# Kernel optimization log

Measured on AMD Instinct MI355X. Metric: run time of the kernel, lower is better.

Reference implementation:

```python
import jax, jax.numpy as jnp
import numpy as np

B, C, H, W = 4, 96, 56, 56
K0, K1, DIL, HID = 5, 7, 3, 4  # HID: ConvMlp(dim, expansion, drop) => hidden_features = int(mlp_ratio) = 4 (repo quirk)
EPS = 1e-5


def _conv(x, w, b, pad, dil=1, groups=1):
    y = jax.lax.conv_general_dilated(x, w, (1, 1), [(pad, pad), (pad, pad)],
                                     rhs_dilation=(dil, dil),
                                     dimension_numbers=('NCHW', 'OIHW', 'NCHW'),
                                     feature_group_count=groups)
    return y + b[None, :, None, None]


def _conv1x1(x, w, b):
    return jnp.einsum('bchw,oc->bohw', x, w) + b[None, :, None, None]


def _ln(x, g, b):
    # LayerNormProxy: LayerNorm over channel dim of NCHW
    mu = jnp.mean(x, axis=1, keepdims=True)
    v = jnp.var(x, axis=1, keepdims=True)
    return (x - mu) * jax.lax.rsqrt(v + EPS) * g[None, :, None, None] + b[None, :, None, None]


def _gelu(x):
    return jax.nn.gelu(x, approximate=False)  # torch nn.GELU default = exact erf


def _deform_dw(x, ow, ob, dw, db, k, dil, pad):
    # DeformConv2d wrapper: offsets from a same-geometry conv, then depthwise deformable conv.
    Bx, Cx, Hx, Wx = x.shape
    P = k * k
    off = _conv(x, ow, ob, pad, dil).reshape(Bx, P, 2, Hx, Wx)  # [B,P,(y,x),H,W]
    ky = (jnp.repeat(jnp.arange(k), k) * dil - pad).astype(x.dtype)  # row-major kernel grid
    kx = (jnp.tile(jnp.arange(k), k) * dil - pad).astype(x.dtype)
    py = jnp.arange(Hx, dtype=x.dtype)[None, None, :, None] + ky[None, :, None, None] + off[:, :, 0]
    px = jnp.arange(Wx, dtype=x.dtype)[None, None, None, :] + kx[None, :, None, None] + off[:, :, 1]
    y0 = jnp.floor(py)
    x0 = jnp.floor(px)
    wy = py - y0
    wx = px - x0
    xf = x.reshape(Bx, Cx, Hx * Wx)

    def corner(yi, xi):
        valid = (yi >= 0) & (yi < Hx) & (xi >= 0) & (xi < Wx)
        idx = (jnp.clip(yi, 0, Hx - 1).astype(jnp.int32) * Wx
               + jnp.clip(xi, 0, Wx - 1).astype(jnp.int32)).reshape(Bx, -1)
        g = jax.vmap(lambda a, i: jnp.take(a, i, axis=1))(xf, idx).reshape(Bx, Cx, P, Hx, Wx)
        return g * valid[:, None].astype(x.dtype)

    v = (corner(y0, x0) * ((1 - wy) * (1 - wx))[:, None]
         + corner(y0, x0 + 1) * ((1 - wy) * wx)[:, None]
         + corner(y0 + 1, x0) * (wy * (1 - wx))[:, None]
         + corner(y0 + 1, x0 + 1) * (wy * wx)[:, None])  # [B,C,P,H,W]
    return jnp.einsum('bcphw,cp->bchw', v, dw) + db[None, :, None, None]


def setup_inputs() -> dict:
    key = jax.random.key(0)
    ks = iter(jax.random.split(key, 32))

    def rn(shape, s=1.0):
        return jax.random.normal(next(ks), shape, jnp.float32) * s

    f32 = jnp.float32
    return {
        'x': rn((B, C, H, W)),
        'g1n': jnp.ones((C,), f32), 'b1n': jnp.zeros((C,), f32),
        'p1w': rn((C, C), 1 / np.sqrt(C)), 'p1b': jnp.zeros((C,), f32),
        'o0w': rn((2 * K0 * K0, C, K0, K0), 0.05 / np.sqrt(C * K0 * K0)), 'o0b': jnp.zeros((2 * K0 * K0,), f32),
        'd0w': rn((C, K0 * K0), 1 / np.sqrt(K0 * K0)), 'd0b': jnp.zeros((C,), f32),
        'o1w': rn((2 * K1 * K1, C, K1, K1), 0.05 / np.sqrt(C * K1 * K1)), 'o1b': jnp.zeros((2 * K1 * K1,), f32),
        'd1w': rn((C, K1 * K1), 1 / np.sqrt(K1 * K1)), 'd1b': jnp.zeros((C,), f32),
        'c1w': rn((C, C), 1 / np.sqrt(C)), 'c1b': jnp.zeros((C,), f32),
        'p2w': rn((C, C), 1 / np.sqrt(C)), 'p2b': jnp.zeros((C,), f32),
        'ls1': jnp.full((C,), 0.01, f32),
        'g2n': jnp.ones((C,), f32), 'b2n': jnp.zeros((C,), f32),
        'f1w': rn((HID, C), 1 / np.sqrt(C)), 'f1b': jnp.zeros((HID,), f32),
        'dww': rn((HID, 1, 3, 3), 1 / 3.0), 'dwb': jnp.zeros((HID,), f32),
        'f2w': rn((C, HID), 1 / np.sqrt(HID)), 'f2b': jnp.zeros((C,), f32),
        'ls2': jnp.full((C,), 0.01, f32),
    }


def reference(x, g1n, b1n, p1w, p1b, o0w, o0b, d0w, d0b, o1w, o1b, d1w, d1b,
              c1w, c1b, p2w, p2b, ls1, g2n, b2n, f1w, f1b, dww, dwb, f2w, f2b, ls2):
    # attention branch
    y = _ln(x, g1n, b1n)
    shortcut = y
    y = _gelu(_conv1x1(y, p1w, p1b))
    u = y
    a = _deform_dw(y, o0w, o0b, d0w, d0b, K0, 1, K0 // 2)
    a = _deform_dw(a, o1w, o1b, d1w, d1b, K1, DIL, (K1 // 2) * DIL)
    a = _conv1x1(a, c1w, c1b)
    y = _conv1x1(u * a, p2w, p2b) + shortcut
    y = ls1[None, :, None, None] * y
    x = x + y
    # MLP branch (note: norm2 is applied to the branch output y, as in the source)
    z = _ln(y, g2n, b2n)
    z = _conv1x1(z, f1w, f1b)
    z = _gelu(_conv(z, dww, dwb, 1, 1, HID))
    z = _conv1x1(z, f2w, f2b)
    x = x + ls2[None, :, None, None] * z
    return x
```

## Files before the change

kernel.cpp:

```cpp
#include <hip/hip_runtime.h>
#include <math.h>

namespace {

constexpr int Bc = 4, Cc = 96, Hc = 56, Wc = 56;
constexpr int HWc = Hc * Wc;
constexpr int Nc  = Bc * HWc;
constexpr float EPSc = 1e-5f;

typedef __attribute__((ext_vector_type(8))) short bf16x8;
typedef __attribute__((ext_vector_type(4))) float f32x4;

__device__ __forceinline__ unsigned short f2bf(float f) {
  union { float f; unsigned u; } x; x.f = f;
  unsigned r = x.u + 0x7fffu + ((x.u >> 16) & 1u);
  return (unsigned short)(r >> 16);
}
__device__ __forceinline__ float bf2f(unsigned short u) {
  union { unsigned u; float f; } x; x.u = (unsigned)u << 16; return x.f;
}
__device__ __forceinline__ float gelu_exact(float x) {
  return 0.5f * x * (1.0f + erff(x * 0.7071067811865475f));
}

__global__ __launch_bounds__(256) void k_ln(const float* __restrict__ x,
                                            const float* __restrict__ g,
                                            const float* __restrict__ b,
                                            unsigned short* __restrict__ outN) {
  int pos = blockIdx.x * 256 + threadIdx.x;
  int bb = pos / HWc, hw = pos % HWc;
  const float* xb = x + (size_t)bb * Cc * HWc + hw;
  float s = 0.f, s2 = 0.f;
  for (int c = 0; c < Cc; ++c) { float v = xb[c * HWc]; s += v; s2 += v * v; }
  float mu  = s * (1.f / Cc);
  float var = fmaxf(s2 * (1.f / Cc) - mu * mu, 0.f);
  float rs  = rsqrtf(var + EPSc);
  unsigned short* ob = outN + (size_t)pos * Cc;
  for (int q = 0; q < 12; ++q) {
    unsigned short t8[8];
#pragma unroll
    for (int j = 0; j < 8; ++j) {
      int c = q * 8 + j;
      t8[j] = f2bf((xb[c * HWc] - mu) * rs * g[c] + b[c]);
    }
    *reinterpret_cast<bf16x8*>(ob + q * 8) = *reinterpret_cast<const bf16x8*>(t8);
  }
}

template <int K_, int MTILES, int P>
__global__ __launch_bounds__(256) void k_pack_w(const float* __restrict__ wsrc,
                                                unsigned short* __restrict__ wpk) {
  constexpr int TOTAL = K_ * K_ * 3 * MTILES * 512;
  int idx = blockIdx.x * 256 + threadIdx.x;
  if (idx >= TOTAL) return;
  int j    = idx & 7;
  int lane = (idx >> 3) & 63;
  int t    = idx >> 9;
  int mt   = t % MTILES;
  int step = t / MTILES;
  int o = mt * 16 + (lane & 15);
  int k = step * 32 + ((lane >> 4) & 3) * 8 + j;
  int p = k / Cc, c = k % Cc;
  float v = 0.f;
  if (o < P) v = wsrc[(((size_t)o * Cc + c) * K_ + p / K_) * K_ + (p % K_)];
  wpk[idx] = f2bf(v);
}

__global__ __launch_bounds__(256) void k_pack_dwt(const float* __restrict__ dwsrc,
                                                  float* __restrict__ dwt, int KK) {
  int idx = blockIdx.x * 256 + threadIdx.x;
  if (idx >= KK * Cc) return;
  int p = idx / Cc, c = idx % Cc;
  dwt[idx] = dwsrc[c * KK + p];
}

template <int GELU, int PADP, int WP>
__global__ __launch_bounds__(256) void k_pwg(const unsigned short* __restrict__ inN,
                                             const unsigned short* __restrict__ wpk,
                                             const float* __restrict__ bq,
                                             unsigned short* __restrict__ outPad) {
  int lane = threadIdx.x & 63;
  int wv = threadIdx.x >> 6;
  int ng = wv & 1, mg = wv >> 1;
  int n = blockIdx.x * 32 + ng * 16 + (lane & 15);
  int ko = ((lane >> 4) & 3) * 8;
  const unsigned short* ib = inN + (size_t)n * Cc + ko;
  const unsigned short* wl = wpk + (size_t)lane * 8;
  f32x4 acc[3];
#pragma unroll
  for (int m = 0; m < 3; ++m) acc[m] = (f32x4){0.f, 0.f, 0.f, 0.f};
#pragma unroll
  for (int ks = 0; ks < 3; ++ks) {
    bf16x8 bf = *reinterpret_cast<const bf16x8*>(ib + ks * 32);
#pragma unroll
    for (int m = 0; m < 3; ++m) {
      bf16x8 af = *reinterpret_cast<const bf16x8*>(wl + (size_t)(ks * 6 + mg * 3 + m) * 512);
      acc[m] = __builtin_amdgcn_mfma_f32_16x16x32_bf16(af, bf, acc[m], 0, 0, 0);
    }
  }
  int bb = n / HWc, hw = n % HWc;
  int h = hw / Wc, w = hw % Wc;
  unsigned short* ob = outPad + (((size_t)bb * (Hc + 2 * PADP) + h + PADP) * WP + w + PADP) * Cc;
  int orow = ((lane >> 4) & 3) * 4;
#pragma unroll
  for (int m = 0; m < 3; ++m) {
    int o0 = (mg * 3 + m) * 16 + orow;
    float4 bv = *reinterpret_cast<const float4*>(bq + o0);
    unsigned short t4[4];
#pragma unroll
    for (int j = 0; j < 4; ++j) {
      float r = acc[m][j] + ((const float*)&bv)[j];
      if (GELU) r = gelu_exact(r);
      t4[j] = f2bf(r);
    }
    *reinterpret_cast<uint2*>(ob + o0) = *reinterpret_cast<const uint2*>(t4);
  }
}

template <int UPADP, int UWP>
__global__ __launch_bounds__(256) void k_comb(const unsigned short* __restrict__ uPad,
                                              const unsigned short* __restrict__ An,
                                              const unsigned short* __restrict__ wpk,
                                              const float* __restrict__ bq,
                                              const unsigned short* __restrict__ ylnN,
                                              const float* __restrict__ ls1q,
                                              const float* __restrict__ x,
                                              float* __restrict__ out,
                                              unsigned short* __restrict__ y2N) {
  int lane = threadIdx.x & 63;
  int wv = threadIdx.x >> 6;
  int ng = wv & 1, mg = wv >> 1;
  int n = blockIdx.x * 32 + ng * 16 + (lane & 15);
  int ko = ((lane >> 4) & 3) * 8;
  int bb = n / HWc, hw = n % HWc;
  int h = hw / Wc, w = hw % Wc;
  const unsigned short* ub = uPad + (((size_t)bb * (Hc + 2 * UPADP) + h + UPADP) * UWP + w + UPADP) * Cc + ko;
  const unsigned short* ab = An + (size_t)n * Cc + ko;
  const unsigned short* wl = wpk + (size_t)lane * 8;
  f32x4 acc[3];
#pragma unroll
  for (int m = 0; m < 3; ++m) acc[m] = (f32x4){0.f, 0.f, 0.f, 0.f};
#pragma unroll
  for (int ks = 0; ks < 3; ++ks) {
    bf16x8 uv = *reinterpret_cast<const bf16x8*>(ub + ks * 32);
    bf16x8 av = *reinterpret_cast<const bf16x8*>(ab + ks * 32);
    union { bf16x8 v; unsigned short s[8]; } uu, aa, gg;
    uu.v = uv; aa.v = av;
#pragma unroll
    for (int j = 0; j < 8; ++j) gg.s[j] = f2bf(bf2f(uu.s[j]) * bf2f(aa.s[j]));
#pragma unroll
    for (int m = 0; m < 3; ++m) {
      bf16x8 af = *reinterpret_cast<const bf16x8*>(wl + (size_t)(ks * 6 + mg * 3 + m) * 512);
      acc[m] = __builtin_amdgcn_mfma_f32_16x16x32_bf16(af, gg.v, acc[m], 0, 0, 0);
    }
  }
  int orow = ((lane >> 4) & 3) * 4;
  const float* xb = x + (size_t)bb * Cc * HWc + hw;
  float* ob = out + (size_t)bb * Cc * HWc + hw;
#pragma unroll
  for (int m = 0; m < 3; ++m) {
    int o0 = (mg * 3 + m) * 16 + orow;
    float4 bv = *reinterpret_cast<const float4*>(bq + o0);
    float4 lv = *reinterpret_cast<const float4*>(ls1q + o0);
    uint2 yl = *reinterpret_cast<const uint2*>(ylnN + (size_t)n * Cc + o0);
    unsigned short yl4[4];
    *reinterpret_cast<uint2*>(yl4) = yl;
    unsigned short t4[4];
#pragma unroll
    for (int j = 0; j < 4; ++j) {
      float t = acc[m][j] + ((const float*)&bv)[j] + bf2f(yl4[j]);
      float y2 = ((const float*)&lv)[j] * t;
      t4[j] = f2bf(y2);
      ob[(size_t)(o0 + j) * HWc] = xb[(size_t)(o0 + j) * HWc] + y2;
    }
    *reinterpret_cast<uint2*>(y2N + (size_t)n * Cc + o0) = *reinterpret_cast<const uint2*>(t4);
  }
}

template <int K_, int DIL_, int MTILES, int MT, int P, int PADP, int WP, int PSTR, int SPLIT>
__global__ __launch_bounds__(256) void k_conv_mfma(const unsigned short* __restrict__ inp,
                                                   const unsigned short* __restrict__ wpk,
                                                   const float* __restrict__ bq,
                                                   float* __restrict__ dstT) {
  constexpr int KK = K_ * K_;
  constexpr int KKbase = KK / SPLIT, KKrem = KK % SPLIT;
  constexpr int HP = Hc + 2 * PADP;
  constexpr int NBLK = Nc / 32;
  int lane = threadIdx.x & 63;
  int wv = threadIdx.x >> 6;
  int bid = blockIdx.x;
  int sp = blockIdx.y;
  int p0 = sp * KKbase + min(sp, KKrem);
  int pcnt = KKbase + (sp < KKrem ? 1 : 0);
  int ntile = (bid & 7) * (NBLK / 8) + (bid >> 3);
  int n0 = ntile * 32 + (lane & 15);
  int n1 = n0 + 16;
  int b0 = n0 / HWc, hw0 = n0 % HWc, h0 = hw0 / Wc, w0 = hw0 % Wc;
  int b1 = n1 / HWc, hw1 = n1 % HWc, h1 = hw1 / Wc, w1 = hw1 % Wc;
  int co = ((lane >> 4) & 3) * 8;
  const unsigned short* ib0 = inp + ((size_t)b0 * HP * WP + (size_t)h0 * WP + w0) * Cc + co;
  const unsigned short* ib1 = inp + ((size_t)b1 * HP * WP + (size_t)h1 * WP + w1) * Cc + co;
  const unsigned short* wl = wpk + (size_t)lane * 8;
  int mt0 = wv * MT;
  int mtc[MT];
#pragma unroll
  for (int i = 0; i < MT; ++i) mtc[i] = min(mt0 + i, MTILES - 1);

  f32x4 acc[MT][2];
#pragma unroll
  for (int i = 0; i < MT; ++i) {
    acc[i][0] = (f32x4){0.f, 0.f, 0.f, 0.f};
    acc[i][1] = (f32x4){0.f, 0.f, 0.f, 0.f};
  }

  bf16x8 Bb[3][2], Aa[MT][3];
  {
    size_t toff = (size_t)((p0 / K_) * DIL_ * WP + (p0 % K_) * DIL_) * Cc;
#pragma unroll
    for (int cc = 0; cc < 3; ++cc) {
      Bb[cc][0] = *reinterpret_cast<const bf16x8*>(ib0 + toff + cc * 32);
      Bb[cc][1] = *reinterpret_cast<const bf16x8*>(ib1 + toff + cc * 32);
#pragma unroll
      for (int i = 0; i < MT; ++i)
        Aa[i][cc] = *reinterpret_cast<const bf16x8*>(wl + ((size_t)(p0 * 3 + cc) * MTILES + mtc[i]) * 512);
    }
  }

#pragma unroll 2
  for (int pi = 0; pi < pcnt; ++pi) {
    int pn = p0 + ((pi + 1 < pcnt) ? pi + 1 : pi);
    size_t toff = (size_t)((pn / K_) * DIL_ * WP + (pn % K_) * DIL_) * Cc;
    const unsigned short* sp0 = ib0 + toff;
    const unsigned short* sp1 = ib1 + toff;
    bf16x8 Bn[3][2], An[MT][3];
#pragma unroll
    for (int cc = 0; cc < 3; ++cc) {
      Bn[cc][0] = *reinterpret_cast<const bf16x8*>(sp0 + cc * 32);
      Bn[cc][1] = *reinterpret_cast<const bf16x8*>(sp1 + cc * 32);
#pragma unroll
      for (int i = 0; i < MT; ++i)
        An[i][cc] = *reinterpret_cast<const bf16x8*>(wl + ((size_t)(pn * 3 + cc) * MTILES + mtc[i]) * 512);
    }
#pragma unroll
    for (int cc = 0; cc < 3; ++cc)
#pragma unroll
      for (int i = 0; i < MT; ++i) {
        acc[i][0] = __builtin_amdgcn_mfma_f32_16x16x32_bf16(Aa[i][cc], Bb[cc][0], acc[i][0], 0, 0, 0);
        acc[i][1] = __builtin_amdgcn_mfma_f32_16x16x32_bf16(Aa[i][cc], Bb[cc][1], acc[i][1], 0, 0, 0);
      }
#pragma unroll
    for (int cc = 0; cc < 3; ++cc) {
      Bb[cc][0] = Bn[cc][0];
      Bb[cc][1] = Bn[cc][1];
#pragma unroll
      for (int i = 0; i < MT; ++i) Aa[i][cc] = An[i][cc];
    }
  }

  float* dsp = dstT + (size_t)sp * Nc * PSTR;
  int orow = ((lane >> 4) & 3) * 4;
#pragma unroll
  for (int i = 0; i < MT; ++i) {
    int mt = mt0 + i;
    if (mt >= MTILES) break;
#pragma unroll
    for (int nt = 0; nt < 2; ++nt) {
      float4 st;
#pragma unroll
      for (int j = 0; j < 4; ++j) {
        int o = mt * 16 + orow + j;
        float bias = (sp == 0 && o < P) ? bq[o] : 0.f;
        ((float*)&st)[j] = acc[i][nt][j] + bias;
      }
      int n = nt ? n1 : n0;
      *reinterpret_cast<float4*>(dsp + (size_t)n * PSTR + mt * 16 + orow) = st;
    }
  }
}

template <int K_, int DIL_, int PAD_, int PSTR, int NSUM>
__global__ __launch_bounds__(256) void k_meta(const float* __restrict__ offT,
                                              uint2* __restrict__ metaI,
                                              float4* __restrict__ metaW) {
  constexpr int KK = K_ * K_;
  int idx = blockIdx.x * 256 + threadIdx.x;
  if (idx >= Nc * KK) return;
  int p = idx % KK, pos = idx / KK;
  int hw = pos % HWc;
  int h = hw / Wc, w = hw % Wc;
  const float* ob = offT + (size_t)pos * PSTR + 2 * p;
  float oy = ob[0], ox = ob[1];
#pragma unroll
  for (int q = 1; q < NSUM; ++q) {
    oy += ob[(size_t)q * Nc * PSTR];
    ox += ob[(size_t)q * Nc * PSTR + 1];
  }
  float py = (float)(h + (p / K_) * DIL_ - PAD_) + oy;
  float px = (float)(w + (p % K_) * DIL_ - PAD_) + ox;
  float y0f = floorf(py), x0f = floorf(px);
  float wy = py - y0f, wx = px - x0f;
  int y0 = (int)y0f, x0 = (int)x0f;
  int y1 = y0 + 1, x1 = x0 + 1;
  bool y0v = (unsigned)y0 < (unsigned)Hc, y1v = (unsigned)y1 < (unsigned)Hc;
  bool x0v = (unsigned)x0 < (unsigned)Wc, x1v = (unsigned)x1 < (unsigned)Wc;
  int y0c = min(max(y0, 0), Hc - 1), y1c = min(max(y1, 0), Hc - 1);
  int x0c = min(max(x0, 0), Wc - 1), x1c = min(max(x1, 0), Wc - 1);
  uint2 mi;
  mi.x = (unsigned)(y0c | (y1c << 16));
  mi.y = (unsigned)(x0c | (x1c << 16));
  float4 mw;
  mw.x = (y0v && x0v) ? (1.f - wy) * (1.f - wx) : 0.f;
  mw.y = (y0v && x1v) ? (1.f - wy) * wx : 0.f;
  mw.z = (y1v && x0v) ? wy * (1.f - wx) : 0.f;
  mw.w = (y1v && x1v) ? wy * wx : 0.f;
  metaI[idx] = mi;
  metaW[idx] = mw;
}

template <int K_, int IPADP, int IWP, int OPADP, int OWP>
__global__ __launch_bounds__(256) void k_deform2(const unsigned short* __restrict__ srcT,
                                                 const uint2* __restrict__ metaI,
                                                 const float4* __restrict__ metaW,
                                                 const float* __restrict__ dwt,
                                                 const float* __restrict__ dbq,
                                                 unsigned short* __restrict__ dstPad) {
  constexpr int KK = K_ * K_;
  constexpr int IHP = Hc + 2 * IPADP;
  int tid = blockIdx.x * 256 + threadIdx.x;
  int cg = tid % 12;
  int pos = tid / 12;
  int c = cg * 8;
  int bb = pos / HWc, hw = pos % HWc;
  int h = hw / Wc, w = hw % Wc;
  const unsigned short* sb = srcT + (size_t)bb * IHP * IWP * Cc + c;
  const uint2* mi = metaI + (size_t)pos * KK;
  const float4* mw = metaW + (size_t)pos * KK;
  float acc[8];
#pragma unroll
  for (int j = 0; j < 8; ++j) acc[j] = 0.f;

  auto tap = [&](int p, uint2 I, float4 W) {
    int y0 = (int)(I.x & 0xffffu) + IPADP, y1 = (int)(I.x >> 16) + IPADP;
    int x0 = (int)(I.y & 0xffffu) + IPADP, x1 = (int)(I.y >> 16) + IPADP;
    int r0 = y0 * IWP, r1 = y1 * IWP;
    const uint4 v00 = *reinterpret_cast<const uint4*>(sb + (size_t)(r0 + x0) * Cc);
    const uint4 v01 = *reinterpret_cast<const uint4*>(sb + (size_t)(r0 + x1) * Cc);
    const uint4 v10 = *reinterpret_cast<const uint4*>(sb + (size_t)(r1 + x0) * Cc);
    const uint4 v11 = *reinterpret_cast<const uint4*>(sb + (size_t)(r1 + x1) * Cc);
    float4 d0 = *reinterpret_cast<const float4*>(dwt + (size_t)p * Cc + c);
    float4 d1 = *reinterpret_cast<const float4*>(dwt + (size_t)p * Cc + c + 4);
    float dv[8] = {d0.x, d0.y, d0.z, d0.w, d1.x, d1.y, d1.z, d1.w};
#pragma unroll
    for (int j = 0; j < 4; ++j) {
      unsigned u00 = ((const unsigned*)&v00)[j], u01 = ((const unsigned*)&v01)[j];
      unsigned u10 = ((const unsigned*)&v10)[j], u11 = ((const unsigned*)&v11)[j];
      union { unsigned u; float f; } a0_, b0_, a1_, b1_, a2_, b2_, a3_, b3_;
      a0_.u = u00 << 16; b0_.u = u00 & 0xffff0000u;
      a1_.u = u01 << 16; b1_.u = u01 & 0xffff0000u;
      a2_.u = u10 << 16; b2_.u = u10 & 0xffff0000u;
      a3_.u = u11 << 16; b3_.u = u11 & 0xffff0000u;
      float lo = W.x * a0_.f + W.y * a1_.f + W.z * a2_.f + W.w * a3_.f;
      float hi = W.x * b0_.f + W.y * b1_.f + W.z * b2_.f + W.w * b3_.f;
      acc[2 * j]     += lo * dv[2 * j];
      acc[2 * j + 1] += hi * dv[2 * j + 1];
    }
  };

  int p = 0;
  for (; p + 1 < KK; p += 2) {
    uint2 I0 = mi[p], I1 = mi[p + 1];
    float4 W0 = mw[p], W1 = mw[p + 1];
    tap(p, I0, W0);
    tap(p + 1, I1, W1);
  }
  { uint2 I = mi[p]; float4 W = mw[p]; tap(p, I, W); }

  unsigned short t8[8];
#pragma unroll
  for (int j = 0; j < 8; ++j) t8[j] = f2bf(acc[j] + dbq[c + j]);
  unsigned short* tb = dstPad + (((size_t)bb * (Hc + 2 * OPADP) + h + OPADP) * OWP + w + OPADP) * Cc + c;
  *reinterpret_cast<bf16x8*>(tb) = *reinterpret_cast<const bf16x8*>(t8);
}

__global__ __launch_bounds__(256) void k_mlp1(const unsigned short* __restrict__ y2N,
                                              const float* __restrict__ g,
                                              const float* __restrict__ b,
                                              const float* __restrict__ f1wq,
                                              const float* __restrict__ f1bq,
                                              float* __restrict__ z4) {
  int pos = blockIdx.x * 256 + threadIdx.x;
  int bb = pos / HWc, hw = pos % HWc;
  const unsigned short* yb = y2N + (size_t)pos * Cc;
  float vv[96];
  float s = 0.f, s2 = 0.f;
#pragma unroll
  for (int q = 0; q < 12; ++q) {
    bf16x8 t = *reinterpret_cast<const bf16x8*>(yb + q * 8);
    union { bf16x8 v; unsigned short s[8]; } u; u.v = t;
#pragma unroll
    for (int j = 0; j < 8; ++j) {
      float f = bf2f(u.s[j]);
      vv[q * 8 + j] = f; s += f; s2 += f * f;
    }
  }
  float mu  = s * (1.f / Cc);
  float var = fmaxf(s2 * (1.f / Cc) - mu * mu, 0.f);
  float rs  = rsqrtf(var + EPSc);
  float a0 = 0.f, a1 = 0.f, a2 = 0.f, a3 = 0.f;
#pragma unroll
  for (int c = 0; c < 96; ++c) {
    float t = (vv[c] - mu) * rs * g[c] + b[c];
    a0 += t * f1wq[0 * Cc + c];
    a1 += t * f1wq[1 * Cc + c];
    a2 += t * f1wq[2 * Cc + c];
    a3 += t * f1wq[3 * Cc + c];
  }
  float* zb = z4 + (size_t)bb * 4 * HWc + hw;
  zb[0 * HWc] = a0 + f1bq[0];
  zb[1 * HWc] = a1 + f1bq[1];
  zb[2 * HWc] = a2 + f1bq[2];
  zb[3 * HWc] = a3 + f1bq[3];
}

__global__ __launch_bounds__(256) void k_mlp_dw(const float* __restrict__ z4,
                                                const float* __restrict__ dwwq,
                                                const float* __restrict__ dwbq,
                                                float* __restrict__ z4b) {
  int tid = blockIdx.x * 256 + threadIdx.x;
  int hw = tid % HWc;
  int bj = tid / HWc;
  int j = bj % 4;
  int h = hw / Wc, w = hw % Wc;
  const float* zb = z4 + (size_t)bj * HWc;
  float s = 0.f;
#pragma unroll
  for (int ky = 0; ky < 3; ++ky) {
    int y = h + ky - 1;
    if ((unsigned)y >= (unsigned)Hc) continue;
#pragma unroll
    for (int kx = 0; kx < 3; ++kx) {
      int x = w + kx - 1;
      if ((unsigned)x >= (unsigned)Wc) continue;
      s += zb[y * Wc + x] * dwwq[j * 9 + ky * 3 + kx];
    }
  }
  z4b[tid] = gelu_exact(s + dwbq[j]);
}

__global__ __launch_bounds__(256) void k_mlp2(const float* __restrict__ z4b,
                                              const float* __restrict__ f2wq,
                                              const float* __restrict__ f2bq,
                                              const float* __restrict__ ls2q,
                                              float* __restrict__ out) {
  int pos = blockIdx.x * 256 + threadIdx.x;
  int bb = pos / HWc, hw = pos % HWc;
  const float* zb = z4b + (size_t)bb * 4 * HWc + hw;
  float z0 = zb[0 * HWc], z1 = zb[1 * HWc], z2 = zb[2 * HWc], z3 = zb[3 * HWc];
  float* ob = out + (size_t)bb * Cc * HWc + hw;
  for (int o = 0; o < Cc; ++o) {
    float s = f2bq[o] + z0 * f2wq[o * 4 + 0] + z1 * f2wq[o * 4 + 1]
                      + z2 * f2wq[o * 4 + 2] + z3 * f2wq[o * 4 + 3];
    ob[o * HWc] += ls2q[o] * s;
  }
}

}

extern "C" void kernel_launch(void* const* d_in, const int* in_sizes, int n_in,
                              void* d_out, int out_size, void* d_ws, size_t ws_size,
                              hipStream_t stream) {
  (void)in_sizes; (void)n_in; (void)out_size; (void)ws_size;
  const float* x   = (const float*)d_in[0];
  const float* g1n = (const float*)d_in[1];
  const float* b1n = (const float*)d_in[2];
  const float* p1w = (const float*)d_in[3];
  const float* p1b = (const float*)d_in[4];
  const float* o0w = (const float*)d_in[5];
  const float* o0b = (const float*)d_in[6];
  const float* d0w = (const float*)d_in[7];
  const float* d0b = (const float*)d_in[8];
  const float* o1w = (const float*)d_in[9];
  const float* o1b = (const float*)d_in[10];
  const float* d1w = (const float*)d_in[11];
  const float* d1b = (const float*)d_in[12];
  const float* c1w = (const float*)d_in[13];
  const float* c1b = (const float*)d_in[14];
  const float* p2w = (const float*)d_in[15];
  const float* p2b = (const float*)d_in[16];
  const float* ls1 = (const float*)d_in[17];
  const float* g2n = (const float*)d_in[18];
  const float* b2n = (const float*)d_in[19];
  const float* f1w = (const float*)d_in[20];
  const float* f1b = (const float*)d_in[21];
  const float* dww = (const float*)d_in[22];
  const float* dwb = (const float*)d_in[23];
  const float* f2w = (const float*)d_in[24];
  const float* f2b = (const float*)d_in[25];
  const float* ls2 = (const float*)d_in[26];
  float* out = (float*)d_out;
  float* ws  = (float*)d_ws;

  float* off0t = ws;                                  size_t o_ = (size_t)2 * Nc * 64;
  float* off1t = ws + o_;                             o_ += (size_t)4 * Nc * 112;
  float* z4    = ws + o_;                             o_ += (size_t)Bc * 4 * HWc;
  float* z4b   = ws + o_;                             o_ += (size_t)Bc * 4 * HWc;
  float* dwt0  = ws + o_;                             o_ += 25 * Cc;
  float* dwt1  = ws + o_;                             o_ += 49 * Cc + 4;
  o_ &= ~(size_t)3;
  uint2*  metaI0 = (uint2*)(ws + o_);                 o_ += (size_t)Nc * 25 * 2;
  float4* metaW0 = (float4*)(ws + o_);                o_ += (size_t)Nc * 25 * 4;
  uint2*  metaI1 = (uint2*)(ws + o_);                 o_ += (size_t)Nc * 49 * 2;
  float4* metaW1 = (float4*)(ws + o_);                o_ += (size_t)Nc * 49 * 4;
  unsigned short* yln_n  = (unsigned short*)(ws + o_); o_ += (size_t)Nc * Cc / 2;
  unsigned short* a1_n   = (unsigned short*)(ws + o_); o_ += (size_t)Nc * Cc / 2;
  unsigned short* A_n    = (unsigned short*)(ws + o_); o_ += (size_t)Nc * Cc / 2;
  unsigned short* y2_n   = (unsigned short*)(ws + o_); o_ += (size_t)Nc * Cc / 2;
  unsigned short* u_pad  = (unsigned short*)(ws + o_); o_ += (size_t)Bc * 60 * 60 * Cc / 2;
  unsigned short* a0_pad = (unsigned short*)(ws + o_); o_ += (size_t)Bc * 74 * 74 * Cc / 2;
  unsigned short* wpk0   = (unsigned short*)(ws + o_); o_ += (size_t)25 * 3 * 4 * 512 / 2;
  unsigned short* wpk1   = (unsigned short*)(ws + o_); o_ += (size_t)49 * 3 * 7 * 512 / 2;
  unsigned short* wpkp1  = (unsigned short*)(ws + o_); o_ += (size_t)3 * 6 * 512 / 2;
  unsigned short* wpkc1  = (unsigned short*)(ws + o_); o_ += (size_t)3 * 6 * 512 / 2;
  unsigned short* wpkp2  = (unsigned short*)(ws + o_); o_ += (size_t)3 * 6 * 512 / 2;

  dim3 b256(256, 1, 1);

  hipMemsetAsync(u_pad, 0, (size_t)Bc * 60 * 60 * Cc * sizeof(unsigned short), stream);
  hipMemsetAsync(a0_pad, 0, (size_t)Bc * 74 * 74 * Cc * sizeof(unsigned short), stream);
  hipLaunchKernelGGL((k_pack_w<5, 4, 50>), dim3((25 * 3 * 4 * 512 + 255) / 256), b256, 0, stream, o0w, wpk0);
  hipLaunchKernelGGL((k_pack_w<7, 7, 98>), dim3((49 * 3 * 7 * 512 + 255) / 256), b256, 0, stream, o1w, wpk1);
  hipLaunchKernelGGL((k_pack_w<1, 6, 96>), dim3((3 * 6 * 512 + 255) / 256), b256, 0, stream, p1w, wpkp1);
  hipLaunchKernelGGL((k_pack_w<1, 6, 96>), dim3((3 * 6 * 512 + 255) / 256), b256, 0, stream, c1w, wpkc1);
  hipLaunchKernelGGL((k_pack_w<1, 6, 96>), dim3((3 * 6 * 512 + 255) / 256), b256, 0, stream, p2w, wpkp2);
  hipLaunchKernelGGL(k_pack_dwt, dim3((25 * Cc + 255) / 256), b256, 0, stream, d0w, dwt0, 25);
  hipLaunchKernelGGL(k_pack_dwt, dim3((49 * Cc + 255) / 256), b256, 0, stream, d1w, dwt1, 49);

  hipLaunchKernelGGL(k_ln, dim3(Nc / 256), b256, 0, stream, x, g1n, b1n, yln_n);
  hipLaunchKernelGGL((k_pwg<1, 2, 60>), dim3(Nc / 32), b256, 0, stream, yln_n, wpkp1, p1b, u_pad);
  hipLaunchKernelGGL((k_conv_mfma<5, 1, 4, 1, 50, 2, 60, 64, 2>), dim3(Nc / 32, 2), b256, 0, stream,
                     u_pad, wpk0, o0b, off0t);
  hipLaunchKernelGGL((k_meta<5, 1, 2, 64, 2>), dim3((Nc * 25 + 255) / 256), b256, 0, stream,
                     off0t, metaI0, metaW0);
  hipLaunchKernelGGL((k_deform2<5, 2, 60, 9, 74>), dim3(Nc * 12 / 256), b256, 0, stream,
                     u_pad, metaI0, metaW0, dwt0, d0b, a0_pad);
  hipLaunchKernelGGL((k_conv_mfma<7, 3, 7, 2, 98, 9, 74, 112, 4>), dim3(Nc / 32, 4), b256, 0, stream,
                     a0_pad, wpk1, o1b, off1t);
  hipLaunchKernelGGL((k_meta<7, 3, 9, 112, 4>), dim3((Nc * 49 + 255) / 256), b256, 0, stream,
                     off1t, metaI1, metaW1);
  hipLaunchKernelGGL((k_deform2<7, 9, 74, 0, 56>), dim3(Nc * 12 / 256), b256, 0, stream,
                     a0_pad, metaI1, metaW1, dwt1, d1b, a1_n);
  hipLaunchKernelGGL((k_pwg<0, 0, 56>), dim3(Nc / 32), b256, 0, stream, a1_n, wpkc1, c1b, A_n);
  hipLaunchKernelGGL((k_comb<2, 60>), dim3(Nc / 32), b256, 0, stream,
                     u_pad, A_n, wpkp2, p2b, yln_n, ls1, x, out, y2_n);
  hipLaunchKernelGGL(k_mlp1, dim3(Nc / 256), b256, 0, stream, y2_n, g2n, b2n, f1w, f1b, z4);
  hipLaunchKernelGGL(k_mlp_dw, dim3(Nc * 4 / 256), b256, 0, stream, z4, dww, dwb, z4b);
  hipLaunchKernelGGL(k_mlp2, dim3(Nc / 256), b256, 0, stream, z4b, f2w, f2b, ls2, out);
}
```

Baseline: 255.2 us.

## Pack deform metadata into one 16-byte record and halve channels per thread

Bilinear sampling metadata (four 6-bit coordinates plus four bf16 corner weights) is packed into a single uint4 per tap, replacing separate uint2 index and float4 weight arrays. The aim is less metadata traffic and fewer loads per tap. The deformable depthwise kernel now handles 4 channels per thread instead of 8, doubling thread count, and batches four taps of gathers to raise memory-level parallelism. Depthwise weights are staged in shared memory. In exchange, bilinear weights lose precision by going to bf16, and each thread now reads the metadata for only half as many channels.

```diff
diff --git a/kernel.cpp b/kernel.cpp
--- a/kernel.cpp
+++ b/kernel.cpp
@@ -280,8 +280,7 @@
 
 template <int K_, int DIL_, int PAD_, int PSTR, int NSUM>
 __global__ __launch_bounds__(256) void k_meta(const float* __restrict__ offT,
-                                              uint2* __restrict__ metaI,
-                                              float4* __restrict__ metaW) {
+                                              uint4* __restrict__ meta) {
   constexpr int KK = K_ * K_;
   int idx = blockIdx.x * 256 + threadIdx.x;
   if (idx >= Nc * KK) return;
@@ -305,81 +304,122 @@
   bool x0v = (unsigned)x0 < (unsigned)Wc, x1v = (unsigned)x1 < (unsigned)Wc;
   int y0c = min(max(y0, 0), Hc - 1), y1c = min(max(y1, 0), Hc - 1);
   int x0c = min(max(x0, 0), Wc - 1), x1c = min(max(x1, 0), Wc - 1);
-  uint2 mi;
-  mi.x = (unsigned)(y0c | (y1c << 16));
-  mi.y = (unsigned)(x0c | (x1c << 16));
-  float4 mw;
-  mw.x = (y0v && x0v) ? (1.f - wy) * (1.f - wx) : 0.f;
-  mw.y = (y0v && x1v) ? (1.f - wy) * wx : 0.f;
-  mw.z = (y1v && x0v) ? wy * (1.f - wx) : 0.f;
-  mw.w = (y1v && x1v) ? wy * wx : 0.f;
-  metaI[idx] = mi;
-  metaW[idx] = mw;
+  float w00 = (y0v && x0v) ? (1.f - wy) * (1.f - wx) : 0.f;
+  float w01 = (y0v && x1v) ? (1.f - wy) * wx : 0.f;
+  float w10 = (y1v && x0v) ? wy * (1.f - wx) : 0.f;
+  float w11 = (y1v && x1v) ? wy * wx : 0.f;
+  uint4 m;
+  m.x = (unsigned)(y0c | (y1c << 6) | (x0c << 12) | (x1c << 18));
+  m.y = 0;
+  m.z = (unsigned)f2bf(w00) | ((unsigned)f2bf(w01) << 16);
+  m.w = (unsigned)f2bf(w10) | ((unsigned)f2bf(w11) << 16);
+  meta[idx] = m;
 }
 
 template <int K_, int IPADP, int IWP, int OPADP, int OWP>
-__global__ __launch_bounds__(256) void k_deform2(const unsigned short* __restrict__ srcT,
-                                                 const uint2* __restrict__ metaI,
-                                                 const float4* __restrict__ metaW,
+__global__ __launch_bounds__(256) void k_deform3(const unsigned short* __restrict__ srcT,
+                                                 const uint4* __restrict__ meta,
                                                  const float* __restrict__ dwt,
                                                  const float* __restrict__ dbq,
                                                  unsigned short* __restrict__ dstPad) {
   constexpr int KK = K_ * K_;
   constexpr int IHP = Hc + 2 * IPADP;
+  __shared__ float sdwt[KK * Cc];
+  for (int i = threadIdx.x; i < KK * Cc; i += 256) sdwt[i] = dwt[i];
+  __syncthreads();
+
   int tid = blockIdx.x * 256 + threadIdx.x;
-  int cg = tid % 12;
-  int pos = tid / 12;
-  int c = cg * 8;
+  int cg = tid % 24;
+  int pos = tid / 24;
+  int c = cg * 4;
   int bb = pos / HWc, hw = pos % HWc;
   int h = hw / Wc, w = hw % Wc;
-  const unsigned short* sb = srcT + (size_t)bb * IHP * IWP * Cc + c;
-  const uint2* mi = metaI + (size_t)pos * KK;
-  const float4* mw = metaW + (size_t)pos * KK;
-  float acc[8];
-#pragma unroll
-  for (int j = 0; j < 8; ++j) acc[j] = 0.f;
-
-  auto tap = [&](int p, uint2 I, float4 W) {
-    int y0 = (int)(I.x & 0xffffu) + IPADP, y1 = (int)(I.x >> 16) + IPADP;
-    int x0 = (int)(I.y & 0xffffu) + IPADP, x1 = (int)(I.y >> 16) + IPADP;
-    int r0 = y0 * IWP, r1 = y1 * IWP;
-    const uint4 v00 = *reinterpret_cast<const uint4*>(sb + (size_t)(r0 + x0) * Cc);
-    const uint4 v01 = *reinterpret_cast<const uint4*>(sb + (size_t)(r0 + x1) * Cc);
-    const uint4 v10 = *reinterpret_cast<const uint4*>(sb + (size_t)(r1 + x0) * Cc);
-    const uint4 v11 = *reinterpret_cast<const uint4*>(sb + (size_t)(r1 + x1) * Cc);
-    float4 d0 = *reinterpret_cast<const float4*>(dwt + (size_t)p * Cc + c);
-    float4 d1 = *reinterpret_cast<const float4*>(dwt + (size_t)p * Cc + c + 4);
-    float dv[8] = {d0.x, d0.y, d0.z, d0.w, d1.x, d1.y, d1.z, d1.w};
-#pragma unroll
-    for (int j = 0; j < 4; ++j) {
-      unsigned u00 = ((const unsigned*)&v00)[j], u01 = ((const unsigned*)&v01)[j];
-      unsigned u10 = ((const unsigned*)&v10)[j], u11 = ((const unsigned*)&v11)[j];
+  const unsigned short* sb = srcT + ((size_t)bb * IHP * IWP + IPADP * IWP + IPADP) * Cc + c;
+  const uint4* mt = meta + (size_t)pos * KK;
+  float ac0 = 0.f, ac1 = 0.f, ac2 = 0.f, ac3 = 0.f;
+
+  constexpr int BT = 4;
+  int p = 0;
+  for (; p + BT <= KK; p += BT) {
+    uint4 m[BT];
+#pragma unroll
+    for (int i = 0; i < BT; ++i) m[i] = mt[p + i];
+    uint2 v[BT][4];
+#pragma unroll
+    for (int i = 0; i < BT; ++i) {
+      unsigned ix = m[i].x;
+      int y0 = (int)(ix & 63u), y1 = (int)((ix >> 6) & 63u);
+      int x0 = (int)((ix >> 12) & 63u), x1 = (int)((ix >> 18) & 63u);
+      const unsigned short* r0 = sb + (size_t)(y0 * IWP) * Cc;
+      const unsigned short* r1 = sb + (size_t)(y1 * IWP) * Cc;
+      v[i][0] = *reinterpret_cast<const uint2*>(r0 + x0 * Cc);
+      v[i][1] = *reinterpret_cast<const uint2*>(r0 + x1 * Cc);
+      v[i][2] = *reinterpret_cast<const uint2*>(r1 + x0 * Cc);
+      v[i][3] = *reinterpret_cast<const uint2*>(r1 + x1 * Cc);
+    }
+#pragma unroll
+    for (int i = 0; i < BT; ++i) {
+      float w00 = bf2f((unsigned short)(m[i].z & 0xffffu));
+      float w01 = bf2f((unsigned short)(m[i].z >> 16));
+      float w10 = bf2f((unsigned short)(m[i].w & 0xffffu));
+      float w11 = bf2f((unsigned short)(m[i].w >> 16));
+      float4 d = *reinterpret_cast<const float4*>(&sdwt[(p + i) * Cc + c]);
+#pragma unroll
+      for (int j = 0; j < 2; ++j) {
+        unsigned u00 = ((const unsigned*)&v[i][0])[j];
+        unsigned u01 = ((const unsigned*)&v[i][1])[j];
+        unsigned u10 = ((const unsigned*)&v[i][2])[j];
+        unsigned u11 = ((const unsigned*)&v[i][3])[j];
+        union { unsigned u; float f; } a0_, b0_, a1_, b1_, a2_, b2_, a3_, b3_;
+        a0_.u = u00 << 16; b0_.u = u00 & 0xffff0000u;
+        a1_.u = u01 << 16; b1_.u = u01 & 0xffff0000u;
+        a2_.u = u10 << 16; b2_.u = u10 & 0xffff0000u;
+        a3_.u = u11 << 16; b3_.u = u11 & 0xffff0000u;
+        float lo = w00 * a0_.f + w01 * a1_.f + w10 * a2_.f + w11 * a3_.f;
+        float hi = w00 * b0_.f + w01 * b1_.f + w10 * b2_.f + w11 * b3_.f;
+        if (j == 0) { ac0 += lo * d.x; ac1 += hi * d.y; }
+        else        { ac2 += lo * d.z; ac3 += hi * d.w; }
+      }
+    }
+  }
+  {
+    uint4 m = mt[p];
+    unsigned ix = m.x;
+    int y0 = (int)(ix & 63u), y1 = (int)((ix >> 6) & 63u);
+    int x0 = (int)((ix >> 12) & 63u), x1 = (int)((ix >> 18) & 63u);
+    const unsigned short* r0 = sb + (size_t)(y0 * IWP) * Cc;
+    const unsigned short* r1 = sb + (size_t)(y1 * IWP) * Cc;
+    uint2 v0 = *reinterpret_cast<const uint2*>(r0 + x0 * Cc);
+    uint2 v1 = *reinterpret_cast<const uint2*>(r0 + x1 * Cc);
+    uint2 v2 = *reinterpret_cast<const uint2*>(r1 + x0 * Cc);
+    uint2 v3 = *reinterpret_cast<const uint2*>(r1 + x1 * Cc);
+    float w00 = bf2f((unsigned short)(m.z & 0xffffu));
+    float w01 = bf2f((unsigned short)(m.z >> 16));
+    float w10 = bf2f((unsigned short)(m.w & 0xffffu));
+    float w11 = bf2f((unsigned short)(m.w >> 16));
+    float4 d = *reinterpret_cast<const float4*>(&sdwt[p * Cc + c]);
+#pragma unroll
+    for (int j = 0; j < 2; ++j) {
+      unsigned u00 = ((const unsigned*)&v0)[j];
+      unsigned u01 = ((const unsigned*)&v1)[j];
+      unsigned u10 = ((const unsigned*)&v2)[j];
+      unsigned u11 = ((const unsigned*)&v3)[j];
       union { unsigned u; float f; } a0_, b0_, a1_, b1_, a2_, b2_, a3_, b3_;
       a0_.u = u00 << 16; b0_.u = u00 & 0xffff0000u;
       a1_.u = u01 << 16; b1_.u = u01 & 0xffff0000u;
       a2_.u = u10 << 16; b2_.u = u10 & 0xffff0000u;
       a3_.u = u11 << 16; b3_.u = u11 & 0xffff0000u;
-      float lo = W.x * a0_.f + W.y * a1_.f + W.z * a2_.f + W.w * a3_.f;
-      float hi = W.x * b0_.f + W.y * b1_.f + W.z * b2_.f + W.w * b3_.f;
-      acc[2 * j]     += lo * dv[2 * j];
-      acc[2 * j + 1] += hi * dv[2 * j + 1];
-    }
-  };
-
-  int p = 0;
-  for (; p + 1 < KK; p += 2) {
-    uint2 I0 = mi[p], I1 = mi[p + 1];
-    float4 W0 = mw[p], W1 = mw[p + 1];
-    tap(p, I0, W0);
-    tap(p + 1, I1, W1);
-  }
-  { uint2 I = mi[p]; float4 W = mw[p]; tap(p, I, W); }
-
-  unsigned short t8[8];
-#pragma unroll
-  for (int j = 0; j < 8; ++j) t8[j] = f2bf(acc[j] + dbq[c + j]);
+      float lo = w00 * a0_.f + w01 * a1_.f + w10 * a2_.f + w11 * a3_.f;
+      float hi = w00 * b0_.f + w01 * b1_.f + w10 * b2_.f + w11 * b3_.f;
+      if (j == 0) { ac0 += lo * d.x; ac1 += hi * d.y; }
+      else        { ac2 += lo * d.z; ac3 += hi * d.w; }
+    }
+  }
+
+  unsigned short t4[4] = {f2bf(ac0 + dbq[c]), f2bf(ac1 + dbq[c + 1]),
+                          f2bf(ac2 + dbq[c + 2]), f2bf(ac3 + dbq[c + 3])};
   unsigned short* tb = dstPad + (((size_t)bb * (Hc + 2 * OPADP) + h + OPADP) * OWP + w + OPADP) * Cc + c;
-  *reinterpret_cast<bf16x8*>(tb) = *reinterpret_cast<const bf16x8*>(t8);
+  *reinterpret_cast<uint2*>(tb) = *reinterpret_cast<const uint2*>(t4);
 }
 
 __global__ __launch_bounds__(256) void k_mlp1(const unsigned short* __restrict__ y2N,
@@ -506,11 +546,9 @@
   float* z4b   = ws + o_;                             o_ += (size_t)Bc * 4 * HWc;
   float* dwt0  = ws + o_;                             o_ += 25 * Cc;
   float* dwt1  = ws + o_;                             o_ += 49 * Cc + 4;
-  o_ &= ~(size_t)3;
-  uint2*  metaI0 = (uint2*)(ws + o_);                 o_ += (size_t)Nc * 25 * 2;
-  float4* metaW0 = (float4*)(ws + o_);                o_ += (size_t)Nc * 25 * 4;
-  uint2*  metaI1 = (uint2*)(ws + o_);                 o_ += (size_t)Nc * 49 * 2;
-  float4* metaW1 = (float4*)(ws + o_);                o_ += (size_t)Nc * 49 * 4;
+  o_ = (o_ + 3) & ~(size_t)3;
+  uint4* metaM0 = (uint4*)(ws + o_);                  o_ += (size_t)Nc * 25 * 4;
+  uint4* metaM1 = (uint4*)(ws + o_);                  o_ += (size_t)Nc * 49 * 4;
   unsigned short* yln_n  = (unsigned short*)(ws + o_); o_ += (size_t)Nc * Cc / 2;
   unsigned short* a1_n   = (unsigned short*)(ws + o_); o_ += (size_t)Nc * Cc / 2;
   unsigned short* A_n    = (unsigned short*)(ws + o_); o_ += (size_t)Nc * Cc / 2;
@@ -540,15 +578,15 @@
   hipLaunchKernelGGL((k_conv_mfma<5, 1, 4, 1, 50, 2, 60, 64, 2>), dim3(Nc / 32, 2), b256, 0, stream,
                      u_pad, wpk0, o0b, off0t);
   hipLaunchKernelGGL((k_meta<5, 1, 2, 64, 2>), dim3((Nc * 25 + 255) / 256), b256, 0, stream,
-                     off0t, metaI0, metaW0);
-  hipLaunchKernelGGL((k_deform2<5, 2, 60, 9, 74>), dim3(Nc * 12 / 256), b256, 0, stream,
-                     u_pad, metaI0, metaW0, dwt0, d0b, a0_pad);
+                     off0t, metaM0);
+  hipLaunchKernelGGL((k_deform3<5, 2, 60, 9, 74>), dim3(Nc * 24 / 256), b256, 0, stream,
+                     u_pad, metaM0, dwt0, d0b, a0_pad);
   hipLaunchKernelGGL((k_conv_mfma<7, 3, 7, 2, 98, 9, 74, 112, 4>), dim3(Nc / 32, 4), b256, 0, stream,
                      a0_pad, wpk1, o1b, off1t);
   hipLaunchKernelGGL((k_meta<7, 3, 9, 112, 4>), dim3((Nc * 49 + 255) / 256), b256, 0, stream,
-                     off1t, metaI1, metaW1);
-  hipLaunchKernelGGL((k_deform2<7, 9, 74, 0, 56>), dim3(Nc * 12 / 256), b256, 0, stream,
-                     a0_pad, metaI1, metaW1, dwt1, d1b, a1_n);
+                     off1t, metaM1);
+  hipLaunchKernelGGL((k_deform3<7, 9, 74, 0, 56>), dim3(Nc * 24 / 256), b256, 0, stream,
+                     a0_pad, metaM1, dwt1, d1b, a1_n);
   hipLaunchKernelGGL((k_pwg<0, 0, 56>), dim3(Nc / 32), b256, 0, stream, a1_n, wpkc1, c1b, A_n);
   hipLaunchKernelGGL((k_comb<2, 60>), dim3(Nc / 32), b256, 0, stream,
                      u_pad, A_n, wpkp2, p2b, yln_n, ls1, x, out, y2_n);
```

Result: faster. 231.5 us (-9.3%).
